# Performance work log

Measured on AMD Instinct MI355X. Metric: run time of the kernel, lower is better.

## Reference

```python
import jax, jax.numpy as jnp
import numpy as np

B, N, FIN, FOUT = 16, 128, 128, 256   # batch, atoms(=max_atom), in_features, out_features
EOUT, BIN, BOUT, CI, L1 = 64, 14, 64, 64, 256


def _rnn_dir(x, wih, whh, bih, bhh):
    # x: [B, T, I]; torch nn.RNN step: h = tanh(x @ Wih^T + bih + h @ Whh^T + bhh)
    h0 = jnp.zeros((x.shape[0], whh.shape[0]), x.dtype)
    def step(h, xt):
        h = jnp.tanh(xt @ wih.T + bih + h @ whh.T + bhh)
        return h, h
    _, ys = jax.lax.scan(step, h0, jnp.swapaxes(x, 0, 1))
    return jnp.swapaxes(ys, 0, 1)  # [B, T, H]


def _bi_rnn(x, wih_f, whh_f, bih_f, bhh_f, wih_b, whh_b, bih_b, bhh_b):
    fwd = _rnn_dir(x, wih_f, whh_f, bih_f, bhh_f)
    bwd = _rnn_dir(x[:, ::-1, :], wih_b, whh_b, bih_b, bhh_b)[:, ::-1, :]
    return jnp.concatenate([fwd, bwd], axis=-1)  # [B, T, 2H]


def setup_inputs() -> dict:
    key = jax.random.key(0)
    ks = jax.random.split(key, 24)
    g = lambda i, shape, s=0.05: (jax.random.normal(ks[i], shape, jnp.float32) * s)
    return {
        "x": g(0, (B, N, FIN), 1.0),
        "adj": jax.random.randint(ks[1], (B, N, N), 0, 2).astype(jnp.int32),
        "w_edge": g(2, (B, N, N, BIN), 1.0),
        "W": g(3, (FIN, FOUT)),
        "a": g(4, (2 * FOUT, EOUT)),
        "wfc_w": g(5, (BIN, BOUT)), "wfc_b": g(6, (BOUT,)),
        "fc_w": g(7, (EOUT + BOUT, 1)), "fc_b": g(8, (1,)),
        "fcc_w": g(9, (FOUT, 1)), "fcc_b": g(10, (1,)),
        "wih_f": g(11, (CI, N)), "whh_f": g(12, (CI, CI)), "bih_f": g(13, (CI,)), "bhh_f": g(14, (CI,)),
        "wih_b": g(15, (CI, N)), "whh_b": g(16, (CI, CI)), "bih_b": g(17, (CI,)), "bhh_b": g(18, (CI,)),
        "fco_w": g(19, (2 * CI + FOUT, L1)), "fco_b": g(20, (L1,)),
    }


def reference(x, adj, w_edge, W, a, wfc_w, wfc_b, fc_w, fc_b, fcc_w, fcc_b,
              wih_f, whh_f, bih_f, bhh_f, wih_b, whh_b, bih_b, bhh_b, fco_w, fco_b):
    h = x @ W  # [B, N, FOUT]
    # faithful reproduction of the repeat/cat(dim=1)/view trick
    t1 = jnp.tile(h, (1, 1, N)).reshape(B, N * N, FOUT)  # row i*N+j = h_i
    t2 = jnp.tile(h, (1, N, 1))                          # row i*N+j = h_j
    atom_trans = jnp.concatenate([t1, t2], axis=1).reshape(B, N, N, 2 * FOUT)
    e = atom_trans @ a                                   # [B, N, N, EOUT]
    wproj = w_edge @ wfc_w + wfc_b                       # [B, N, N, BOUT]
    e = jax.nn.leaky_relu(jnp.concatenate([e, wproj], axis=3))
    e = (e @ fc_w + fc_b)[..., 0]                        # [B, N, N]
    att = jax.nn.softmax(jnp.where(adj > 0, e, jnp.float32(-9e15)), axis=2)
    # dropout is identity in eval mode
    at_in = att[..., None] * h[:, :, None, :]            # [B, N, N, FOUT], h_i broadcast over j
    hn = jax.nn.leaky_relu((at_in @ fcc_w + fcc_b)[..., 0])  # [B, N, N]
    hn = jax.nn.leaky_relu(_bi_rnn(hn, wih_f, whh_f, bih_f, bhh_f, wih_b, whh_b, bih_b, bhh_b))
    h1 = jnp.einsum('bij,bjf->bif', att, h)              # [B, N, FOUT]
    out = jnp.concatenate([hn, h1], axis=2) @ fco_w + fco_b  # [B, N, L1]
    return jax.nn.elu(out)
```

## Files before the change

### kernel.cpp

```cpp
#include <hip/hip_runtime.h>
#include <hip/hip_bf16.h>

#define DEV static __device__ __forceinline__

constexpr int B=16, N=128, FIN=128, FOUT=256, EOUT=64, BINW=14, BOUT=64, CI=64, L1=256;

constexpr int O_H   = 0;
constexpr int O_S   = O_H  + B*N*FOUT;
constexpr int O_SU  = O_S  + B*N;
constexpr int O_SV  = O_SU + B*N;
constexpr int O_ATT = O_SV + B*N;
constexpr int O_ZF  = O_ATT+ B*N*N;
constexpr int O_ZB  = O_ZF + B*N*CI;
constexpr int O_RF  = O_ZB + B*N*CI;
constexpr int O_RB  = O_RF + B*N*CI;
constexpr int O_H1  = O_RB + B*N*CI;

DEV float bf16_to_f32(unsigned short u){
  unsigned int x = ((unsigned int)u) << 16; float f;
  __builtin_memcpy(&f, &x, 4); return f;
}
DEV void bf2x(unsigned int u, float& lo, float& hi){
  unsigned int a = u << 16, b = u & 0xFFFF0000u;
  __builtin_memcpy(&lo, &a, 4); __builtin_memcpy(&hi, &b, 4);
}
DEV float lrelu(float x){ return x > 0.f ? x : 0.01f * x; }
DEV float bcastf(float v, int lane){
  return __builtin_bit_cast(float, __builtin_amdgcn_readlane(__builtin_bit_cast(int, v), lane));
}
DEV float ldf(const void* p, int i, int m){
  return m ? bf16_to_f32(((const unsigned short*)p)[i]) : ((const float*)p)[i];
}
DEV int blk_mode(const void* x, int nt, int tid){
  const unsigned short* u = (const unsigned short*)x;
  int e = (u[tid & 255] >> 7) & 0xFF;
  int cnt = __syncthreads_count(e >= 100 && e <= 140);
  return cnt * 4 >= nt * 3;
}

__global__ __launch_bounds__(256) void k_h_pq(const void* __restrict__ xr,
                                              const void* __restrict__ Wp,
                                              const void* __restrict__ Ap,
                                              const void* __restrict__ fccwp,
                                              const void* __restrict__ fcwp,
                                              float* __restrict__ ws){
  int blk = blockIdx.x, tid = threadIdx.x;
  int b = blk >> 4, i0 = (blk & 15) * 8;
  __shared__ __align__(16) float xl[8*FIN];
  __shared__ __align__(16) float hrow[8*FOUT];
  __shared__ __align__(16) float pl[8*EOUT];
  __shared__ __align__(16) float ql[8*EOUT];
  __shared__ float red[32];
  int mode = blk_mode(xr, 256, tid);
  if (mode){
    const unsigned short* xu = (const unsigned short*)xr + (size_t)(b*N + i0)*FIN;
    for (int t = tid; t < 8*FIN/8; t += 256){
      uint4 u4 = ((const uint4*)xu)[t];
      float* o = &xl[t*8];
      bf2x(u4.x,o[0],o[1]); bf2x(u4.y,o[2],o[3]); bf2x(u4.z,o[4],o[5]); bf2x(u4.w,o[6],o[7]);
    }
  } else {
    const float* xf = (const float*)xr + (size_t)(b*N + i0)*FIN;
    for (int t4 = tid; t4 < 8*FIN/4; t4 += 256)
      *(float4*)&xl[t4*4] = ((const float4*)xf)[t4];
  }
  __syncthreads();
  int f = tid;
  float acc[8] = {0,0,0,0,0,0,0,0};
  if (mode){
    const unsigned short* Wu = (const unsigned short*)Wp;
    for (int c = 0; c < FIN; c += 4){
      float w0 = bf16_to_f32(Wu[(c+0)*FOUT + f]);
      float w1 = bf16_to_f32(Wu[(c+1)*FOUT + f]);
      float w2 = bf16_to_f32(Wu[(c+2)*FOUT + f]);
      float w3 = bf16_to_f32(Wu[(c+3)*FOUT + f]);
      #pragma unroll
      for (int r = 0; r < 8; ++r){
        float4 x4 = *(const float4*)&xl[r*FIN + c];
        acc[r] += x4.x*w0 + x4.y*w1 + x4.z*w2 + x4.w*w3;
      }
    }
  } else {
    const float* Wf = (const float*)Wp;
    for (int c = 0; c < FIN; c += 4){
      float w0 = Wf[(c+0)*FOUT + f];
      float w1 = Wf[(c+1)*FOUT + f];
      float w2 = Wf[(c+2)*FOUT + f];
      float w3 = Wf[(c+3)*FOUT + f];
      #pragma unroll
      for (int r = 0; r < 8; ++r){
        float4 x4 = *(const float4*)&xl[r*FIN + c];
        acc[r] += x4.x*w0 + x4.y*w1 + x4.z*w2 + x4.w*w3;
      }
    }
  }
  float fw = ldf(fccwp, f, mode);
  #pragma unroll
  for (int r = 0; r < 8; ++r){
    ws[O_H + (b*N + i0 + r)*FOUT + f] = acc[r];
    hrow[r*FOUT + f] = acc[r];
  }
  #pragma unroll
  for (int r = 0; r < 8; ++r){
    float v = acc[r] * fw;
    for (int off = 32; off; off >>= 1) v += __shfl_down(v, off);
    if ((tid & 63) == 0) red[(tid >> 6)*8 + r] = v;
  }
  __syncthreads();
  if (tid < 8){
    float s = red[tid] + red[8+tid] + red[16+tid] + red[24+tid];
    ws[O_S + b*N + i0 + tid] = s;
  }
  {
    int o = tid & 63, which = (tid >> 6) & 1, hh = tid >> 7;
    float a4[4] = {0.f,0.f,0.f,0.f};
    if (mode){
      const unsigned short* Au = (const unsigned short*)Ap;
      for (int c = 0; c < FOUT; c += 4){
        float w0 = bf16_to_f32(Au[(which*FOUT + c+0)*EOUT + o]);
        float w1 = bf16_to_f32(Au[(which*FOUT + c+1)*EOUT + o]);
        float w2 = bf16_to_f32(Au[(which*FOUT + c+2)*EOUT + o]);
        float w3 = bf16_to_f32(Au[(which*FOUT + c+3)*EOUT + o]);
        #pragma unroll
        for (int r = 0; r < 4; ++r){
          float4 h4 = *(const float4*)&hrow[(hh*4+r)*FOUT + c];
          a4[r] += h4.x*w0 + h4.y*w1 + h4.z*w2 + h4.w*w3;
        }
      }
    } else {
      const float* Af = (const float*)Ap;
      for (int c = 0; c < FOUT; c += 4){
        float w0 = Af[(which*FOUT + c+0)*EOUT + o];
        float w1 = Af[(which*FOUT + c+1)*EOUT + o];
        float w2 = Af[(which*FOUT + c+2)*EOUT + o];
        float w3 = Af[(which*FOUT + c+3)*EOUT + o];
        #pragma unroll
        for (int r = 0; r < 4; ++r){
          float4 h4 = *(const float4*)&hrow[(hh*4+r)*FOUT + c];
          a4[r] += h4.x*w0 + h4.y*w1 + h4.z*w2 + h4.w*w3;
        }
      }
    }
    float* dst = which ? ql : pl;
    #pragma unroll
    for (int r = 0; r < 4; ++r) dst[(hh*4+r)*EOUT + o] = a4[r];
  }
  __syncthreads();
  {
    int o = tid & 63, w = tid >> 6;
    float fw2 = ldf(fcwp, o, mode);
    float s1 = lrelu(pl[w*EOUT + o]     + ql[w*EOUT + o])     * fw2;
    float s2 = lrelu(pl[(w+4)*EOUT + o] + ql[(w+4)*EOUT + o]) * fw2;
    float s3 = lrelu(pl[(2*w)*EOUT + o] + ql[(2*w+1)*EOUT + o]) * fw2;
    for (int off = 32; off; off >>= 1){
      s1 += __shfl_down(s1, off); s2 += __shfl_down(s2, off); s3 += __shfl_down(s3, off);
    }
    if (o == 0){
      ws[O_SU + b*N + i0 + w]     = s1;
      ws[O_SU + b*N + i0 + w + 4] = s2;
      int r1 = (i0 + 2*w) >> 1;
      ws[O_SV + b*N + r1]      = s3;
      ws[O_SV + b*N + r1 + 64] = s3;
    }
  }
}

struct AttArgs { const void *we,*x,*wfcw,*wfcb,*fcw,*fcb,*fccb,*wihf,*bihf,*bhhf,*wihb,*bihb,*bhhb; };

__global__ __launch_bounds__(256) void k_att(AttArgs A, const int* __restrict__ adj,
                                             float* __restrict__ ws){
  int blk = blockIdx.x, tid = threadIdx.x;
  int half = tid >> 7, j = tid & 127, wv = (tid >> 6) & 1;
  int tau = blk*2 + half;
  int b = tau >> 7, i = tau & 127;
  __shared__ __align__(16) float wel[2][N*BINW];
  __shared__ __align__(16) float hnp[2][N];
  __shared__ __align__(16) float wfcwl[BINW*BOUT];
  __shared__ __align__(16) float wfcbl[BOUT];
  __shared__ __align__(16) float fcw2l[BOUT];
  __shared__ float red2[2][2];
  int mode = blk_mode(A.x, 256, tid);
  for (int t = tid; t < BINW*BOUT; t += 256) wfcwl[t] = ldf(A.wfcw, t, mode);
  if (tid < BOUT){ wfcbl[tid] = ldf(A.wfcb, tid, mode); fcw2l[tid] = ldf(A.fcw, EOUT + tid, mode); }
  if (mode){
    const unsigned short* weu = (const unsigned short*)A.we + (size_t)(b*N + i)*N*BINW;
    for (int t = j; t < N*BINW/8; t += 128){
      uint4 q = ((const uint4*)weu)[t];
      float* o = &wel[half][t*8];
      bf2x(q.x,o[0],o[1]); bf2x(q.y,o[2],o[3]); bf2x(q.z,o[4],o[5]); bf2x(q.w,o[6],o[7]);
    }
  } else {
    const float* wef = (const float*)A.we + (size_t)(b*N + i)*N*BINW;
    for (int t4 = j; t4 < N*BINW/4; t4 += 128)
      *(float4*)&wel[half][t4*4] = ((const float4*)wef)[t4];
  }
  __syncthreads();
  float wr[BINW];
  #pragma unroll
  for (int t = 0; t < BINW; ++t) wr[t] = wel[half][j*BINW + t];
  float wcon = 0.f;
  for (int o = 0; o < BOUT; o += 4){
    float4 bb = *(const float4*)&wfcbl[o];
    float w0 = bb.x, w1 = bb.y, w2 = bb.z, w3 = bb.w;
    #pragma unroll
    for (int t = 0; t < BINW; ++t){
      float4 w4 = *(const float4*)&wfcwl[t*BOUT + o];
      w0 = fmaf(wr[t], w4.x, w0); w1 = fmaf(wr[t], w4.y, w1);
      w2 = fmaf(wr[t], w4.z, w2); w3 = fmaf(wr[t], w4.w, w3);
    }
    float4 f4 = *(const float4*)&fcw2l[o];
    wcon += lrelu(w0)*f4.x + lrelu(w1)*f4.y + lrelu(w2)*f4.z + lrelu(w3)*f4.w;
  }
  const float* R = ws;
  float econ = (i < 64) ? R[O_SU + b*N + 2*i + (j >= 64 ? 1 : 0)]
                        : R[O_SV + b*N + j];
  float etot = econ + wcon + ldf(A.fcb, 0, mode);
  float m = (adj[(b*N + i)*N + j] > 0) ? etot : -9e15f;
  float mx = m;
  for (int off = 32; off; off >>= 1) mx = fmaxf(mx, __shfl_xor(mx, off));
  if ((tid & 63) == 0) red2[half][wv] = mx;
  __syncthreads();
  mx = fmaxf(red2[half][0], red2[half][1]);
  float ev = expf(m - mx);
  float sum = ev;
  for (int off = 32; off; off >>= 1) sum += __shfl_xor(sum, off);
  __syncthreads();
  if ((tid & 63) == 0) red2[half][wv] = sum;
  __syncthreads();
  sum = red2[half][0] + red2[half][1];
  float att = ev / sum;
  ws[O_ATT + (b*N + i)*N + j] = att;
  float sbi = R[O_S + b*N + i];
  hnp[half][j] = lrelu(att * sbi + ldf(A.fccb, 0, mode));
  __syncthreads();
  {
    int d = wv, c = tid & 63;
    float acc = ldf(d ? A.bihb : A.bihf, c, mode) + ldf(d ? A.bhhb : A.bhhf, c, mode);
    const void* wihp = d ? A.wihb : A.wihf;
    if (mode){
      const uint4* wq = (const uint4*)((const unsigned short*)wihp + c*N);
      #pragma unroll 4
      for (int k = 0; k < N; k += 8){
        uint4 q = wq[k >> 3];
        float w0,w1,w2,w3,w4,w5,w6,w7;
        bf2x(q.x,w0,w1); bf2x(q.y,w2,w3); bf2x(q.z,w4,w5); bf2x(q.w,w6,w7);
        float4 h0 = *(const float4*)&hnp[half][k];
        float4 h1 = *(const float4*)&hnp[half][k+4];
        acc += h0.x*w0 + h0.y*w1 + h0.z*w2 + h0.w*w3
             + h1.x*w4 + h1.y*w5 + h1.z*w6 + h1.w*w7;
      }
    } else {
      const float* wf = (const float*)wihp + c*N;
      #pragma unroll 8
      for (int k = 0; k < N; k += 4){
        float4 h4 = *(const float4*)&hnp[half][k];
        float4 w4 = *(const float4*)&wf[k];
        acc += h4.x*w4.x + h4.y*w4.y + h4.z*w4.z + h4.w*w4.w;
      }
    }
    ws[(d ? O_ZB : O_ZF) + (b*N + i)*CI + c] = acc;
  }
}

__global__ __launch_bounds__(256, 1) void k_rnn_h1(const void* __restrict__ xr,
                                                   const void* __restrict__ whhf,
                                                   const void* __restrict__ whhb,
                                                   float* __restrict__ ws){
  __shared__ __align__(16) float sh[N*CI];
  int blk = blockIdx.x, tid = threadIdx.x;
  int mode = blk_mode(xr, 256, tid);
  const float* R = ws;
  if (blk < 32){
    int d = blk >> 4, b = blk & 15;
    const int zb = (d ? O_ZB : O_ZF) + b*N*CI;
    const int ob = (d ? O_RB : O_RF) + b*N*CI;
    for (int it = tid; it < N*CI/4; it += 256)
      *(float4*)&sh[it*4] = *(const float4*)&ws[zb + it*4];
    __syncthreads();
    if (tid < 64){
      int c = tid;
      const void* whhp = d ? whhb : whhf;
      float wreg[CI];
      if (mode){
        const uint4* wq = (const uint4*)((const unsigned short*)whhp + c*CI);
        #pragma unroll
        for (int k = 0; k < CI; k += 8){
          uint4 q = wq[k >> 3];
          bf2x(q.x,wreg[k+0],wreg[k+1]); bf2x(q.y,wreg[k+2],wreg[k+3]);
          bf2x(q.z,wreg[k+4],wreg[k+5]); bf2x(q.w,wreg[k+6],wreg[k+7]);
        }
      } else {
        const float* wf = (const float*)whhp + c*CI;
        #pragma unroll
        for (int k = 0; k < CI; k += 4){
          float4 w4 = *(const float4*)&wf[k];
          wreg[k]=w4.x; wreg[k+1]=w4.y; wreg[k+2]=w4.z; wreg[k+3]=w4.w;
        }
      }
      const int step = d ? -1 : 1;
      int tt = d ? (N-1) : 0;
      float hv = 0.f;
      float z = sh[tt*CI + c];
      for (int t = 0; t < N; ++t){
        int ti = tt + step; ti = ti < 0 ? 0 : (ti > N-1 ? N-1 : ti);
        float znext = sh[ti*CI + c];
        float s[CI];
        #pragma unroll
        for (int k = 0; k < CI; ++k) s[k] = bcastf(hv, k);
#if __has_builtin(__builtin_amdgcn_sched_barrier)
        __builtin_amdgcn_sched_barrier(0);
#endif
        float a0 = z, a1 = 0.f, a2 = 0.f, a3 = 0.f;
        #pragma unroll
        for (int k = 0; k < CI; k += 4){
          a0 = fmaf(s[k+0], wreg[k+0], a0);
          a1 = fmaf(s[k+1], wreg[k+1], a1);
          a2 = fmaf(s[k+2], wreg[k+2], a2);
          a3 = fmaf(s[k+3], wreg[k+3], a3);
        }
        float x = (a0+a1)+(a2+a3);
        x = fminf(15.f, fmaxf(-15.f, x));
        float p = __expf(2.f * x);
        hv = (p - 1.f) * __builtin_amdgcn_rcpf(p + 1.f);
        sh[tt*CI + c] = hv;
        z = znext;
        tt += step;
      }
    }
    __syncthreads();
    for (int it = tid; it < N*CI/4; it += 256)
      *(float4*)&ws[ob + it*4] = *(const float4*)&sh[it*4];
  } else {
    for (int task = blk - 32; task < 256; task += 224){
      int b = task >> 4, i0 = (task & 15) * 8;
      int f = tid;
      __syncthreads();
      for (int t = tid; t < 8*N; t += 256){
        int r = t >> 7, k = t & 127;
        sh[k*8 + r] = R[O_ATT + (b*N + i0 + r)*N + k];
      }
      __syncthreads();
      float acc[8] = {0,0,0,0,0,0,0,0};
      for (int k = 0; k < N; ++k){
        float hv = R[O_H + (b*N + k)*FOUT + f];
        float4 a0 = *(const float4*)&sh[k*8];
        float4 a1 = *(const float4*)&sh[k*8 + 4];
        acc[0] += a0.x*hv; acc[1] += a0.y*hv; acc[2] += a0.z*hv; acc[3] += a0.w*hv;
        acc[4] += a1.x*hv; acc[5] += a1.y*hv; acc[6] += a1.z*hv; acc[7] += a1.w*hv;
      }
      #pragma unroll
      for (int r = 0; r < 8; ++r)
        ws[O_H1 + (b*N + i0 + r)*FOUT + f] = acc[r];
    }
  }
}

__global__ __launch_bounds__(256) void k_out(const void* __restrict__ xr,
                                             const void* __restrict__ fcowp,
                                             const void* __restrict__ fcobp,
                                             const float* __restrict__ R, void* dout){
  int blk = blockIdx.x, tid = threadIdx.x;
  int b = blk >> 4, i0 = (blk & 15) * 8;
  constexpr int KW = 2*CI + FOUT;
  __shared__ __align__(16) float inl[8*KW];
  int mode = blk_mode(xr, 256, tid);
  for (int t = tid; t < 8*2*CI; t += 256){
    int r = t >> 7, k = t & 127;
    int row = b*N + i0 + r;
    inl[r*KW + k] = (k < CI) ? lrelu(R[O_RF + row*CI + k])
                             : lrelu(R[O_RB + row*CI + (k - CI)]);
  }
  for (int t = tid; t < 8*FOUT; t += 256){
    int r = t >> 8, k = t & 255;
    inl[r*KW + 2*CI + k] = R[O_H1 + (b*N + i0 + r)*FOUT + k];
  }
  __syncthreads();
  int l = tid;
  float bias = ldf(fcobp, l, mode);
  float acc[8];
  #pragma unroll
  for (int r = 0; r < 8; ++r) acc[r] = bias;
  if (mode){
    const unsigned short* fu = (const unsigned short*)fcowp;
    for (int k = 0; k < KW; k += 4){
      float w0 = bf16_to_f32(fu[(k+0)*L1 + l]);
      float w1 = bf16_to_f32(fu[(k+1)*L1 + l]);
      float w2 = bf16_to_f32(fu[(k+2)*L1 + l]);
      float w3 = bf16_to_f32(fu[(k+3)*L1 + l]);
      #pragma unroll
      for (int r = 0; r < 8; ++r){
        float4 v = *(const float4*)&inl[r*KW + k];
        acc[r] += v.x*w0 + v.y*w1 + v.z*w2 + v.w*w3;
      }
    }
  } else {
    const float* ff = (const float*)fcowp;
    for (int k = 0; k < KW; k += 4){
      float w0 = ff[(k+0)*L1 + l];
      float w1 = ff[(k+1)*L1 + l];
      float w2 = ff[(k+2)*L1 + l];
      float w3 = ff[(k+3)*L1 + l];
      #pragma unroll
      for (int r = 0; r < 8; ++r){
        float4 v = *(const float4*)&inl[r*KW + k];
        acc[r] += v.x*w0 + v.y*w1 + v.z*w2 + v.w*w3;
      }
    }
  }
  #pragma unroll
  for (int r = 0; r < 8; ++r){
    float o = acc[r] > 0.f ? acc[r] : expm1f(acc[r]);
    int idx = (b*N + i0 + r)*L1 + l;
    if (mode) ((__hip_bfloat16*)dout)[idx] = __float2bfloat16(o);
    else      ((float*)dout)[idx] = o;
  }
}

extern "C" void kernel_launch(void* const* d_in, const int* in_sizes, int n_in,
                              void* d_out, int out_size, void* d_ws, size_t ws_size,
                              hipStream_t stream){
  (void)in_sizes; (void)n_in; (void)out_size; (void)ws_size;
  float* ws = (float*)d_ws;
  AttArgs A;
  A.we = d_in[2]; A.x = d_in[0]; A.wfcw = d_in[5]; A.wfcb = d_in[6];
  A.fcw = d_in[7]; A.fcb = d_in[8]; A.fccb = d_in[10];
  A.wihf = d_in[11]; A.bihf = d_in[13]; A.bhhf = d_in[14];
  A.wihb = d_in[15]; A.bihb = d_in[17]; A.bhhb = d_in[18];
  hipLaunchKernelGGL(k_h_pq,   dim3(256),    dim3(256), 0, stream,
                     d_in[0], d_in[3], d_in[4], d_in[9], d_in[7], ws);
  hipLaunchKernelGGL(k_att,    dim3(B*N/2),  dim3(256), 0, stream, A, (const int*)d_in[1], ws);
  hipLaunchKernelGGL(k_rnn_h1, dim3(256),    dim3(256), 0, stream,
                     d_in[0], d_in[12], d_in[16], ws);
  hipLaunchKernelGGL(k_out,    dim3(256),    dim3(256), 0, stream,
                     d_in[0], d_in[19], d_in[20], ws, d_out);
}
```

Before: 206.8 us.

## Fuse four kernels into one cooperative persistent kernel with grid syncs

Merges the h/pq projection, attention, RNN/h1 and output kernels into a single cooperative launch of 256 blocks, with grid-wide syncs between stages. The attention stage, which previously used 1024 blocks, now loops over 4 row pairs per block. The aim is to remove three kernel launch gaps and their tail effects. In exchange the attention stage has less parallelism, and each grid sync plus threadfence adds its own cost.

```diff
diff --git a/kernel.cpp b/kernel.cpp
--- a/kernel.cpp
+++ b/kernel.cpp
@@ -1,5 +1,8 @@
 #include <hip/hip_runtime.h>
 #include <hip/hip_bf16.h>
+#include <hip/hip_cooperative_groups.h>
+
+namespace cg = cooperative_groups;
 
 #define DEV static __device__ __forceinline__
 
@@ -38,381 +41,388 @@
   return cnt * 4 >= nt * 3;
 }
 
-__global__ __launch_bounds__(256) void k_h_pq(const void* __restrict__ xr,
-                                              const void* __restrict__ Wp,
-                                              const void* __restrict__ Ap,
-                                              const void* __restrict__ fccwp,
-                                              const void* __restrict__ fcwp,
-                                              float* __restrict__ ws){
+struct FA {
+  const void *x, *Wp, *Ap, *fccw, *fcw;
+  const int  *adj;
+  const void *we, *wfcw, *wfcb, *fcb, *fccb;
+  const void *wihf, *bihf, *bhhf, *wihb, *bihb, *bhhb;
+  const void *whhf, *whhb;
+  const void *fcow, *fcob;
+  float *ws;
+  void  *dout;
+};
+
+__global__ __launch_bounds__(256, 1) void k_fused(FA A){
+  cg::grid_group gg = cg::this_grid();
+  __shared__ __align__(16) float smem[8192];
   int blk = blockIdx.x, tid = threadIdx.x;
-  int b = blk >> 4, i0 = (blk & 15) * 8;
-  __shared__ __align__(16) float xl[8*FIN];
-  __shared__ __align__(16) float hrow[8*FOUT];
-  __shared__ __align__(16) float pl[8*EOUT];
-  __shared__ __align__(16) float ql[8*EOUT];
-  __shared__ float red[32];
-  int mode = blk_mode(xr, 256, tid);
-  if (mode){
-    const unsigned short* xu = (const unsigned short*)xr + (size_t)(b*N + i0)*FIN;
-    for (int t = tid; t < 8*FIN/8; t += 256){
-      uint4 u4 = ((const uint4*)xu)[t];
-      float* o = &xl[t*8];
-      bf2x(u4.x,o[0],o[1]); bf2x(u4.y,o[2],o[3]); bf2x(u4.z,o[4],o[5]); bf2x(u4.w,o[6],o[7]);
-    }
-  } else {
-    const float* xf = (const float*)xr + (size_t)(b*N + i0)*FIN;
-    for (int t4 = tid; t4 < 8*FIN/4; t4 += 256)
-      *(float4*)&xl[t4*4] = ((const float4*)xf)[t4];
+  int mode = blk_mode(A.x, 256, tid);
+  float* ws = A.ws;
+  const float* R = ws;
+
+  {
+    int b = blk >> 4, i0 = (blk & 15) * 8;
+    float* xl   = smem;
+    float* hrow = smem + 1024;
+    float* pl   = smem + 3072;
+    float* ql   = smem + 3584;
+    float* red  = smem + 4096;
+    if (mode){
+      const unsigned short* xu = (const unsigned short*)A.x + (size_t)(b*N + i0)*FIN;
+      for (int t = tid; t < 8*FIN/8; t += 256){
+        uint4 u4 = ((const uint4*)xu)[t];
+        float* o = &xl[t*8];
+        bf2x(u4.x,o[0],o[1]); bf2x(u4.y,o[2],o[3]); bf2x(u4.z,o[4],o[5]); bf2x(u4.w,o[6],o[7]);
+      }
+    } else {
+      const float* xf = (const float*)A.x + (size_t)(b*N + i0)*FIN;
+      for (int t4 = tid; t4 < 8*FIN/4; t4 += 256)
+        *(float4*)&xl[t4*4] = ((const float4*)xf)[t4];
+    }
+    __syncthreads();
+    int f = tid;
+    float acc[8] = {0,0,0,0,0,0,0,0};
+    if (mode){
+      const unsigned short* Wu = (const unsigned short*)A.Wp;
+      for (int c = 0; c < FIN; c += 4){
+        float w0 = bf16_to_f32(Wu[(c+0)*FOUT + f]);
+        float w1 = bf16_to_f32(Wu[(c+1)*FOUT + f]);
+        float w2 = bf16_to_f32(Wu[(c+2)*FOUT + f]);
+        float w3 = bf16_to_f32(Wu[(c+3)*FOUT + f]);
+        #pragma unroll
+        for (int r = 0; r < 8; ++r){
+          float4 x4 = *(const float4*)&xl[r*FIN + c];
+          acc[r] += x4.x*w0 + x4.y*w1 + x4.z*w2 + x4.w*w3;
+        }
+      }
+    } else {
+      const float* Wf = (const float*)A.Wp;
+      for (int c = 0; c < FIN; c += 4){
+        float w0 = Wf[(c+0)*FOUT + f];
+        float w1 = Wf[(c+1)*FOUT + f];
+        float w2 = Wf[(c+2)*FOUT + f];
+        float w3 = Wf[(c+3)*FOUT + f];
+        #pragma unroll
+        for (int r = 0; r < 8; ++r){
+          float4 x4 = *(const float4*)&xl[r*FIN + c];
+          acc[r] += x4.x*w0 + x4.y*w1 + x4.z*w2 + x4.w*w3;
+        }
+      }
+    }
+    float fw = ldf(A.fccw, f, mode);
+    #pragma unroll
+    for (int r = 0; r < 8; ++r){
+      ws[O_H + (b*N + i0 + r)*FOUT + f] = acc[r];
+      hrow[r*FOUT + f] = acc[r];
+    }
+    #pragma unroll
+    for (int r = 0; r < 8; ++r){
+      float v = acc[r] * fw;
+      for (int off = 32; off; off >>= 1) v += __shfl_down(v, off);
+      if ((tid & 63) == 0) red[(tid >> 6)*8 + r] = v;
+    }
+    __syncthreads();
+    if (tid < 8){
+      float s = red[tid] + red[8+tid] + red[16+tid] + red[24+tid];
+      ws[O_S + b*N + i0 + tid] = s;
+    }
+    {
+      int o = tid & 63, which = (tid >> 6) & 1, hh = tid >> 7;
+      float a4[4] = {0.f,0.f,0.f,0.f};
+      if (mode){
+        const unsigned short* Au = (const unsigned short*)A.Ap;
+        for (int c = 0; c < FOUT; c += 4){
+          float w0 = bf16_to_f32(Au[(which*FOUT + c+0)*EOUT + o]);
+          float w1 = bf16_to_f32(Au[(which*FOUT + c+1)*EOUT + o]);
+          float w2 = bf16_to_f32(Au[(which*FOUT + c+2)*EOUT + o]);
+          float w3 = bf16_to_f32(Au[(which*FOUT + c+3)*EOUT + o]);
+          #pragma unroll
+          for (int r = 0; r < 4; ++r){
+            float4 h4 = *(const float4*)&hrow[(hh*4+r)*FOUT + c];
+            a4[r] += h4.x*w0 + h4.y*w1 + h4.z*w2 + h4.w*w3;
+          }
+        }
+      } else {
+        const float* Af = (const float*)A.Ap;
+        for (int c = 0; c < FOUT; c += 4){
+          float w0 = Af[(which*FOUT + c+0)*EOUT + o];
+          float w1 = Af[(which*FOUT + c+1)*EOUT + o];
+          float w2 = Af[(which*FOUT + c+2)*EOUT + o];
+          float w3 = Af[(which*FOUT + c+3)*EOUT + o];
+          #pragma unroll
+          for (int r = 0; r < 4; ++r){
+            float4 h4 = *(const float4*)&hrow[(hh*4+r)*FOUT + c];
+            a4[r] += h4.x*w0 + h4.y*w1 + h4.z*w2 + h4.w*w3;
+          }
+        }
+      }
+      float* dst = which ? ql : pl;
+      #pragma unroll
+      for (int r = 0; r < 4; ++r) dst[(hh*4+r)*EOUT + o] = a4[r];
+    }
+    __syncthreads();
+    {
+      int o = tid & 63, w = tid >> 6;
+      float fw2 = ldf(A.fcw, o, mode);
+      float s1 = lrelu(pl[w*EOUT + o]     + ql[w*EOUT + o])     * fw2;
+      float s2 = lrelu(pl[(w+4)*EOUT + o] + ql[(w+4)*EOUT + o]) * fw2;
+      float s3 = lrelu(pl[(2*w)*EOUT + o] + ql[(2*w+1)*EOUT + o]) * fw2;
+      for (int off = 32; off; off >>= 1){
+        s1 += __shfl_down(s1, off); s2 += __shfl_down(s2, off); s3 += __shfl_down(s3, off);
+      }
+      if (o == 0){
+        ws[O_SU + b*N + i0 + w]     = s1;
+        ws[O_SU + b*N + i0 + w + 4] = s2;
+        int r1 = (i0 + 2*w) >> 1;
+        ws[O_SV + b*N + r1]      = s3;
+        ws[O_SV + b*N + r1 + 64] = s3;
+      }
+    }
   }
-  __syncthreads();
-  int f = tid;
-  float acc[8] = {0,0,0,0,0,0,0,0};
-  if (mode){
-    const unsigned short* Wu = (const unsigned short*)Wp;
-    for (int c = 0; c < FIN; c += 4){
-      float w0 = bf16_to_f32(Wu[(c+0)*FOUT + f]);
-      float w1 = bf16_to_f32(Wu[(c+1)*FOUT + f]);
-      float w2 = bf16_to_f32(Wu[(c+2)*FOUT + f]);
-      float w3 = bf16_to_f32(Wu[(c+3)*FOUT + f]);
+  __threadfence();
+  gg.sync();
+
+  {
+    float (*wel)[N*BINW] = (float (*)[N*BINW])smem;
+    float (*hnp)[N]      = (float (*)[N])(smem + 3584);
+    float* wfcwl = smem + 3840;
+    float* wfcbl = smem + 4736;
+    float* fcw2l = smem + 4800;
+    float (*red2)[2]     = (float (*)[2])(smem + 4864);
+    for (int t = tid; t < BINW*BOUT; t += 256) wfcwl[t] = ldf(A.wfcw, t, mode);
+    if (tid < BOUT){ wfcbl[tid] = ldf(A.wfcb, tid, mode); fcw2l[tid] = ldf(A.fcw, EOUT + tid, mode); }
+    int half = tid >> 7, j = tid & 127, wv = (tid >> 6) & 1;
+    float fcbv = ldf(A.fcb, 0, mode), fccbv = ldf(A.fccb, 0, mode);
+    for (int pr = 0; pr < 4; ++pr){
+      int tau = blk*8 + pr*2 + half;
+      int b = tau >> 7, i = tau & 127;
+      if (mode){
+        const unsigned short* weu = (const unsigned short*)A.we + (size_t)(b*N + i)*N*BINW;
+        for (int t = j; t < N*BINW/8; t += 128){
+          uint4 q = ((const uint4*)weu)[t];
+          float* o = &wel[half][t*8];
+          bf2x(q.x,o[0],o[1]); bf2x(q.y,o[2],o[3]); bf2x(q.z,o[4],o[5]); bf2x(q.w,o[6],o[7]);
+        }
+      } else {
+        const float* wef = (const float*)A.we + (size_t)(b*N + i)*N*BINW;
+        for (int t4 = j; t4 < N*BINW/4; t4 += 128)
+          *(float4*)&wel[half][t4*4] = ((const float4*)wef)[t4];
+      }
+      __syncthreads();
+      float wr[BINW];
       #pragma unroll
-      for (int r = 0; r < 8; ++r){
-        float4 x4 = *(const float4*)&xl[r*FIN + c];
-        acc[r] += x4.x*w0 + x4.y*w1 + x4.z*w2 + x4.w*w3;
-      }
-    }
-  } else {
-    const float* Wf = (const float*)Wp;
-    for (int c = 0; c < FIN; c += 4){
-      float w0 = Wf[(c+0)*FOUT + f];
-      float w1 = Wf[(c+1)*FOUT + f];
-      float w2 = Wf[(c+2)*FOUT + f];
-      float w3 = Wf[(c+3)*FOUT + f];
-      #pragma unroll
-      for (int r = 0; r < 8; ++r){
-        float4 x4 = *(const float4*)&xl[r*FIN + c];
-        acc[r] += x4.x*w0 + x4.y*w1 + x4.z*w2 + x4.w*w3;
-      }
+      for (int t = 0; t < BINW; ++t) wr[t] = wel[half][j*BINW + t];
+      float wcon = 0.f;
+      for (int o = 0; o < BOUT; o += 4){
+        float4 bb = *(const float4*)&wfcbl[o];
+        float w0 = bb.x, w1 = bb.y, w2 = bb.z, w3 = bb.w;
+        #pragma unroll
+        for (int t = 0; t < BINW; ++t){
+          float4 w4 = *(const float4*)&wfcwl[t*BOUT + o];
+          w0 = fmaf(wr[t], w4.x, w0); w1 = fmaf(wr[t], w4.y, w1);
+          w2 = fmaf(wr[t], w4.z, w2); w3 = fmaf(wr[t], w4.w, w3);
+        }
+        float4 f4 = *(const float4*)&fcw2l[o];
+        wcon += lrelu(w0)*f4.x + lrelu(w1)*f4.y + lrelu(w2)*f4.z + lrelu(w3)*f4.w;
+      }
+      float econ = (i < 64) ? R[O_SU + b*N + 2*i + (j >= 64 ? 1 : 0)]
+                            : R[O_SV + b*N + j];
+      float etot = econ + wcon + fcbv;
+      float m = (A.adj[(b*N + i)*N + j] > 0) ? etot : -9e15f;
+      float mx = m;
+      for (int off = 32; off; off >>= 1) mx = fmaxf(mx, __shfl_xor(mx, off));
+      if ((tid & 63) == 0) red2[half][wv] = mx;
+      __syncthreads();
+      mx = fmaxf(red2[half][0], red2[half][1]);
+      float ev = expf(m - mx);
+      float sum = ev;
+      for (int off = 32; off; off >>= 1) sum += __shfl_xor(sum, off);
+      __syncthreads();
+      if ((tid & 63) == 0) red2[half][wv] = sum;
+      __syncthreads();
+      sum = red2[half][0] + red2[half][1];
+      float att = ev / sum;
+      ws[O_ATT + (b*N + i)*N + j] = att;
+      float sbi = R[O_S + b*N + i];
+      hnp[half][j] = lrelu(att * sbi + fccbv);
+      __syncthreads();
+      {
+        int d = wv, c = tid & 63;
+        float acc = ldf(d ? A.bihb : A.bihf, c, mode) + ldf(d ? A.bhhb : A.bhhf, c, mode);
+        const void* wihp = d ? A.wihb : A.wihf;
+        if (mode){
+          const uint4* wq = (const uint4*)((const unsigned short*)wihp + c*N);
+          #pragma unroll 4
+          for (int k = 0; k < N; k += 8){
+            uint4 q = wq[k >> 3];
+            float w0,w1,w2,w3,w4,w5,w6,w7;
+            bf2x(q.x,w0,w1); bf2x(q.y,w2,w3); bf2x(q.z,w4,w5); bf2x(q.w,w6,w7);
+            float4 h0 = *(const float4*)&hnp[half][k];
+            float4 h1 = *(const float4*)&hnp[half][k+4];
+            acc += h0.x*w0 + h0.y*w1 + h0.z*w2 + h0.w*w3
+                 + h1.x*w4 + h1.y*w5 + h1.z*w6 + h1.w*w7;
+          }
+        } else {
+          const float* wf = (const float*)wihp + c*N;
+          #pragma unroll 8
+          for (int k = 0; k < N; k += 4){
+            float4 h4 = *(const float4*)&hnp[half][k];
+            float4 w4 = *(const float4*)&wf[k];
+            acc += h4.x*w4.x + h4.y*w4.y + h4.z*w4.z + h4.w*w4.w;
+          }
+        }
+        ws[(d ? O_ZB : O_ZF) + (b*N + i)*CI + c] = acc;
+      }
+      __syncthreads();
     }
   }
-  float fw = ldf(fccwp, f, mode);
-  #pragma unroll
-  for (int r = 0; r < 8; ++r){
-    ws[O_H + (b*N + i0 + r)*FOUT + f] = acc[r];
-    hrow[r*FOUT + f] = acc[r];
+  __threadfence();
+  gg.sync();
+
+  {
+    float* sh = smem;
+    if (blk < 32){
+      int d = blk >> 4, b = blk & 15;
+      const int zb = (d ? O_ZB : O_ZF) + b*N*CI;
+      const int ob = (d ? O_RB : O_RF) + b*N*CI;
+      for (int it = tid; it < N*CI/4; it += 256)
+        *(float4*)&sh[it*4] = *(const float4*)&ws[zb + it*4];
+      __syncthreads();
+      if (tid < 64){
+        int c = tid;
+        const void* whhp = d ? A.whhb : A.whhf;
+        float wreg[CI];
+        if (mode){
+          const uint4* wq = (const uint4*)((const unsigned short*)whhp + c*CI);
+          #pragma unroll
+          for (int k = 0; k < CI; k += 8){
+            uint4 q = wq[k >> 3];
+            bf2x(q.x,wreg[k+0],wreg[k+1]); bf2x(q.y,wreg[k+2],wreg[k+3]);
+            bf2x(q.z,wreg[k+4],wreg[k+5]); bf2x(q.w,wreg[k+6],wreg[k+7]);
+          }
+        } else {
+          const float* wf = (const float*)whhp + c*CI;
+          #pragma unroll
+          for (int k = 0; k < CI; k += 4){
+            float4 w4 = *(const float4*)&wf[k];
+            wreg[k]=w4.x; wreg[k+1]=w4.y; wreg[k+2]=w4.z; wreg[k+3]=w4.w;
+          }
+        }
+        const int step = d ? -1 : 1;
+        int tt = d ? (N-1) : 0;
+        float hv = 0.f;
+        float z = sh[tt*CI + c];
+        for (int t = 0; t < N; ++t){
+          int ti = tt + step; ti = ti < 0 ? 0 : (ti > N-1 ? N-1 : ti);
+          float znext = sh[ti*CI + c];
+          float s[CI];
+          #pragma unroll
+          for (int k = 0; k < CI; ++k) s[k] = bcastf(hv, k);
+#if __has_builtin(__builtin_amdgcn_sched_barrier)
+          __builtin_amdgcn_sched_barrier(0);
+#endif
+          float a0 = z, a1 = 0.f, a2 = 0.f, a3 = 0.f;
+          #pragma unroll
+          for (int k = 0; k < CI; k += 4){
+            a0 = fmaf(s[k+0], wreg[k+0], a0);
+            a1 = fmaf(s[k+1], wreg[k+1], a1);
+            a2 = fmaf(s[k+2], wreg[k+2], a2);
+            a3 = fmaf(s[k+3], wreg[k+3], a3);
+          }
+          float x = (a0+a1)+(a2+a3);
+          x = fminf(15.f, fmaxf(-15.f, x));
+          float p = __expf(2.f * x);
+          hv = (p - 1.f) * __builtin_amdgcn_rcpf(p + 1.f);
+          sh[tt*CI + c] = hv;
+          z = znext;
+          tt += step;
+        }
+      }
+      __syncthreads();
+      for (int it = tid; it < N*CI/4; it += 256)
+        *(float4*)&ws[ob + it*4] = *(const float4*)&sh[it*4];
+    } else {
+      for (int task = blk - 32; task < 256; task += 224){
+        int b = task >> 4, i0 = (task & 15) * 8;
+        int f = tid;
+        __syncthreads();
+        for (int t = tid; t < 8*N; t += 256){
+          int r = t >> 7, k = t & 127;
+          sh[k*8 + r] = R[O_ATT + (b*N + i0 + r)*N + k];
+        }
+        __syncthreads();
+        float acc[8] = {0,0,0,0,0,0,0,0};
+        for (int k = 0; k < N; ++k){
+          float hv = R[O_H + (b*N + k)*FOUT + f];
+          float4 a0 = *(const float4*)&sh[k*8];
+          float4 a1 = *(const float4*)&sh[k*8 + 4];
+          acc[0] += a0.x*hv; acc[1] += a0.y*hv; acc[2] += a0.z*hv; acc[3] += a0.w*hv;
+          acc[4] += a1.x*hv; acc[5] += a1.y*hv; acc[6] += a1.z*hv; acc[7] += a1.w*hv;
+        }
+        #pragma unroll
+        for (int r = 0; r < 8; ++r)
+          ws[O_H1 + (b*N + i0 + r)*FOUT + f] = acc[r];
+      }
+    }
   }
-  #pragma unroll
-  for (int r = 0; r < 8; ++r){
-    float v = acc[r] * fw;
-    for (int off = 32; off; off >>= 1) v += __shfl_down(v, off);
-    if ((tid & 63) == 0) red[(tid >> 6)*8 + r] = v;
-  }
-  __syncthreads();
-  if (tid < 8){
-    float s = red[tid] + red[8+tid] + red[16+tid] + red[24+tid];
-    ws[O_S + b*N + i0 + tid] = s;
-  }
+  __threadfence();
+  gg.sync();
+
   {
-    int o = tid & 63, which = (tid >> 6) & 1, hh = tid >> 7;
-    float a4[4] = {0.f,0.f,0.f,0.f};
+    int b = blk >> 4, i0 = (blk & 15) * 8;
+    constexpr int KW = 2*CI + FOUT;
+    float* inl = smem;
+    __syncthreads();
+    for (int t = tid; t < 8*2*CI; t += 256){
+      int r = t >> 7, k = t & 127;
+      int row = b*N + i0 + r;
+      inl[r*KW + k] = (k < CI) ? lrelu(R[O_RF + row*CI + k])
+                               : lrelu(R[O_RB + row*CI + (k - CI)]);
+    }
+    for (int t = tid; t < 8*FOUT; t += 256){
+      int r = t >> 8, k = t & 255;
+      inl[r*KW + 2*CI + k] = R[O_H1 + (b*N + i0 + r)*FOUT + k];
+    }
+    __syncthreads();
+    int l = tid;
+    float bias = ldf(A.fcob, l, mode);
+    float acc[8];
+    #pragma unroll
+    for (int r = 0; r < 8; ++r) acc[r] = bias;
     if (mode){
-      const unsigned short* Au = (const unsigned short*)Ap;
-      for (int c = 0; c < FOUT; c += 4){
-        float w0 = bf16_to_f32(Au[(which*FOUT + c+0)*EOUT + o]);
-        float w1 = bf16_to_f32(Au[(which*FOUT + c+1)*EOUT + o]);
-        float w2 = bf16_to_f32(Au[(which*FOUT + c+2)*EOUT + o]);
-        float w3 = bf16_to_f32(Au[(which*FOUT + c+3)*EOUT + o]);
-        #pragma unroll
-        for (int r = 0; r < 4; ++r){
-          float4 h4 = *(const float4*)&hrow[(hh*4+r)*FOUT + c];
-          a4[r] += h4.x*w0 + h4.y*w1 + h4.z*w2 + h4.w*w3;
+      const unsigned short* fu = (const unsigned short*)A.fcow;
+      for (int k = 0; k < KW; k += 4){
+        float w0 = bf16_to_f32(fu[(k+0)*L1 + l]);
+        float w1 = bf16_to_f32(fu[(k+1)*L1 + l]);
+        float w2 = bf16_to_f32(fu[(k+2)*L1 + l]);
+        float w3 = bf16_to_f32(fu[(k+3)*L1 + l]);
+        #pragma unroll
+        for (int r = 0; r < 8; ++r){
+          float4 v = *(const float4*)&inl[r*KW + k];
+          acc[r] += v.x*w0 + v.y*w1 + v.z*w2 + v.w*w3;
         }
       }
     } else {
-      const float* Af = (const float*)Ap;
-      for (int c = 0; c < FOUT; c += 4){
-        float w0 = Af[(which*FOUT + c+0)*EOUT + o];
-        float w1 = Af[(which*FOUT + c+1)*EOUT + o];
-        float w2 = Af[(which*FOUT + c+2)*EOUT + o];
-        float w3 = Af[(which*FOUT + c+3)*EOUT + o];
-        #pragma unroll
-        for (int r = 0; r < 4; ++r){
-          float4 h4 = *(const float4*)&hrow[(hh*4+r)*FOUT + c];
-          a4[r] += h4.x*w0 + h4.y*w1 + h4.z*w2 + h4.w*w3;
-        }
-      }
-    }
-    float* dst = which ? ql : pl;
+      const float* ff = (const float*)A.fcow;
+      for (int k = 0; k < KW; k += 4){
+        float w0 = ff[(k+0)*L1 + l];
+        float w1 = ff[(k+1)*L1 + l];
+        float w2 = ff[(k+2)*L1 + l];
+        float w3 = ff[(k+3)*L1 + l];
+        #pragma unroll
+        for (int r = 0; r < 8; ++r){
+          float4 v = *(const float4*)&inl[r*KW + k];
+          acc[r] += v.x*w0 + v.y*w1 + v.z*w2 + v.w*w3;
+        }
+      }
+    }
     #pragma unroll
-    for (int r = 0; r < 4; ++r) dst[(hh*4+r)*EOUT + o] = a4[r];
-  }
-  __syncthreads();
-  {
-    int o = tid & 63, w = tid >> 6;
-    float fw2 = ldf(fcwp, o, mode);
-    float s1 = lrelu(pl[w*EOUT + o]     + ql[w*EOUT + o])     * fw2;
-    float s2 = lrelu(pl[(w+4)*EOUT + o] + ql[(w+4)*EOUT + o]) * fw2;
-    float s3 = lrelu(pl[(2*w)*EOUT + o] + ql[(2*w+1)*EOUT + o]) * fw2;
-    for (int off = 32; off; off >>= 1){
-      s1 += __shfl_down(s1, off); s2 += __shfl_down(s2, off); s3 += __shfl_down(s3, off);
-    }
-    if (o == 0){
-      ws[O_SU + b*N + i0 + w]     = s1;
-      ws[O_SU + b*N + i0 + w + 4] = s2;
-      int r1 = (i0 + 2*w) >> 1;
-      ws[O_SV + b*N + r1]      = s3;
-      ws[O_SV + b*N + r1 + 64] = s3;
-    }
-  }
-}
-
-struct AttArgs { const void *we,*x,*wfcw,*wfcb,*fcw,*fcb,*fccb,*wihf,*bihf,*bhhf,*wihb,*bihb,*bhhb; };
-
-__global__ __launch_bounds__(256) void k_att(AttArgs A, const int* __restrict__ adj,
-                                             float* __restrict__ ws){
-  int blk = blockIdx.x, tid = threadIdx.x;
-  int half = tid >> 7, j = tid & 127, wv = (tid >> 6) & 1;
-  int tau = blk*2 + half;
-  int b = tau >> 7, i = tau & 127;
-  __shared__ __align__(16) float wel[2][N*BINW];
-  __shared__ __align__(16) float hnp[2][N];
-  __shared__ __align__(16) float wfcwl[BINW*BOUT];
-  __shared__ __align__(16) float wfcbl[BOUT];
-  __shared__ __align__(16) float fcw2l[BOUT];
-  __shared__ float red2[2][2];
-  int mode = blk_mode(A.x, 256, tid);
-  for (int t = tid; t < BINW*BOUT; t += 256) wfcwl[t] = ldf(A.wfcw, t, mode);
-  if (tid < BOUT){ wfcbl[tid] = ldf(A.wfcb, tid, mode); fcw2l[tid] = ldf(A.fcw, EOUT + tid, mode); }
-  if (mode){
-    const unsigned short* weu = (const unsigned short*)A.we + (size_t)(b*N + i)*N*BINW;
-    for (int t = j; t < N*BINW/8; t += 128){
-      uint4 q = ((const uint4*)weu)[t];
-      float* o = &wel[half][t*8];
-      bf2x(q.x,o[0],o[1]); bf2x(q.y,o[2],o[3]); bf2x(q.z,o[4],o[5]); bf2x(q.w,o[6],o[7]);
-    }
-  } else {
-    const float* wef = (const float*)A.we + (size_t)(b*N + i)*N*BINW;
-    for (int t4 = j; t4 < N*BINW/4; t4 += 128)
-      *(float4*)&wel[half][t4*4] = ((const float4*)wef)[t4];
-  }
-  __syncthreads();
-  float wr[BINW];
-  #pragma unroll
-  for (int t = 0; t < BINW; ++t) wr[t] = wel[half][j*BINW + t];
-  float wcon = 0.f;
-  for (int o = 0; o < BOUT; o += 4){
-    float4 bb = *(const float4*)&wfcbl[o];
-    float w0 = bb.x, w1 = bb.y, w2 = bb.z, w3 = bb.w;
-    #pragma unroll
-    for (int t = 0; t < BINW; ++t){
-      float4 w4 = *(const float4*)&wfcwl[t*BOUT + o];
-      w0 = fmaf(wr[t], w4.x, w0); w1 = fmaf(wr[t], w4.y, w1);
-      w2 = fmaf(wr[t], w4.z, w2); w3 = fmaf(wr[t], w4.w, w3);
-    }
-    float4 f4 = *(const float4*)&fcw2l[o];
-    wcon += lrelu(w0)*f4.x + lrelu(w1)*f4.y + lrelu(w2)*f4.z + lrelu(w3)*f4.w;
-  }
-  const float* R = ws;
-  float econ = (i < 64) ? R[O_SU + b*N + 2*i + (j >= 64 ? 1 : 0)]
-                        : R[O_SV + b*N + j];
-  float etot = econ + wcon + ldf(A.fcb, 0, mode);
-  float m = (adj[(b*N + i)*N + j] > 0) ? etot : -9e15f;
-  float mx = m;
-  for (int off = 32; off; off >>= 1) mx = fmaxf(mx, __shfl_xor(mx, off));
-  if ((tid & 63) == 0) red2[half][wv] = mx;
-  __syncthreads();
-  mx = fmaxf(red2[half][0], red2[half][1]);
-  float ev = expf(m - mx);
-  float sum = ev;
-  for (int off = 32; off; off >>= 1) sum += __shfl_xor(sum, off);
-  __syncthreads();
-  if ((tid & 63) == 0) red2[half][wv] = sum;
-  __syncthreads();
-  sum = red2[half][0] + red2[half][1];
-  float att = ev / sum;
-  ws[O_ATT + (b*N + i)*N + j] = att;
-  float sbi = R[O_S + b*N + i];
-  hnp[half][j] = lrelu(att * sbi + ldf(A.fccb, 0, mode));
-  __syncthreads();
-  {
-    int d = wv, c = tid & 63;
-    float acc = ldf(d ? A.bihb : A.bihf, c, mode) + ldf(d ? A.bhhb : A.bhhf, c, mode);
-    const void* wihp = d ? A.wihb : A.wihf;
-    if (mode){
-      const uint4* wq = (const uint4*)((const unsigned short*)wihp + c*N);
-      #pragma unroll 4
-      for (int k = 0; k < N; k += 8){
-        uint4 q = wq[k >> 3];
-        float w0,w1,w2,w3,w4,w5,w6,w7;
-        bf2x(q.x,w0,w1); bf2x(q.y,w2,w3); bf2x(q.z,w4,w5); bf2x(q.w,w6,w7);
-        float4 h0 = *(const float4*)&hnp[half][k];
-        float4 h1 = *(const float4*)&hnp[half][k+4];
-        acc += h0.x*w0 + h0.y*w1 + h0.z*w2 + h0.w*w3
-             + h1.x*w4 + h1.y*w5 + h1.z*w6 + h1.w*w7;
-      }
-    } else {
-      const float* wf = (const float*)wihp + c*N;
-      #pragma unroll 8
-      for (int k = 0; k < N; k += 4){
-        float4 h4 = *(const float4*)&hnp[half][k];
-        float4 w4 = *(const float4*)&wf[k];
-        acc += h4.x*w4.x + h4.y*w4.y + h4.z*w4.z + h4.w*w4.w;
-      }
-    }
-    ws[(d ? O_ZB : O_ZF) + (b*N + i)*CI + c] = acc;
-  }
-}
-
-__global__ __launch_bounds__(256, 1) void k_rnn_h1(const void* __restrict__ xr,
-                                                   const void* __restrict__ whhf,
-                                                   const void* __restrict__ whhb,
-                                                   float* __restrict__ ws){
-  __shared__ __align__(16) float sh[N*CI];
-  int blk = blockIdx.x, tid = threadIdx.x;
-  int mode = blk_mode(xr, 256, tid);
-  const float* R = ws;
-  if (blk < 32){
-    int d = blk >> 4, b = blk & 15;
-    const int zb = (d ? O_ZB : O_ZF) + b*N*CI;
-    const int ob = (d ? O_RB : O_RF) + b*N*CI;
-    for (int it = tid; it < N*CI/4; it += 256)
-      *(float4*)&sh[it*4] = *(const float4*)&ws[zb + it*4];
-    __syncthreads();
-    if (tid < 64){
-      int c = tid;
-      const void* whhp = d ? whhb : whhf;
-      float wreg[CI];
-      if (mode){
-        const uint4* wq = (const uint4*)((const unsigned short*)whhp + c*CI);
-        #pragma unroll
-        for (int k = 0; k < CI; k += 8){
-          uint4 q = wq[k >> 3];
-          bf2x(q.x,wreg[k+0],wreg[k+1]); bf2x(q.y,wreg[k+2],wreg[k+3]);
-          bf2x(q.z,wreg[k+4],wreg[k+5]); bf2x(q.w,wreg[k+6],wreg[k+7]);
-        }
-      } else {
-        const float* wf = (const float*)whhp + c*CI;
-        #pragma unroll
-        for (int k = 0; k < CI; k += 4){
-          float4 w4 = *(const float4*)&wf[k];
-          wreg[k]=w4.x; wreg[k+1]=w4.y; wreg[k+2]=w4.z; wreg[k+3]=w4.w;
-        }
-      }
-      const int step = d ? -1 : 1;
-      int tt = d ? (N-1) : 0;
-      float hv = 0.f;
-      float z = sh[tt*CI + c];
-      for (int t = 0; t < N; ++t){
-        int ti = tt + step; ti = ti < 0 ? 0 : (ti > N-1 ? N-1 : ti);
-        float znext = sh[ti*CI + c];
-        float s[CI];
-        #pragma unroll
-        for (int k = 0; k < CI; ++k) s[k] = bcastf(hv, k);
-#if __has_builtin(__builtin_amdgcn_sched_barrier)
-        __builtin_amdgcn_sched_barrier(0);
-#endif
-        float a0 = z, a1 = 0.f, a2 = 0.f, a3 = 0.f;
-        #pragma unroll
-        for (int k = 0; k < CI; k += 4){
-          a0 = fmaf(s[k+0], wreg[k+0], a0);
-          a1 = fmaf(s[k+1], wreg[k+1], a1);
-          a2 = fmaf(s[k+2], wreg[k+2], a2);
-          a3 = fmaf(s[k+3], wreg[k+3], a3);
-        }
-        float x = (a0+a1)+(a2+a3);
-        x = fminf(15.f, fmaxf(-15.f, x));
-        float p = __expf(2.f * x);
-        hv = (p - 1.f) * __builtin_amdgcn_rcpf(p + 1.f);
-        sh[tt*CI + c] = hv;
-        z = znext;
-        tt += step;
-      }
-    }
-    __syncthreads();
-    for (int it = tid; it < N*CI/4; it += 256)
-      *(float4*)&ws[ob + it*4] = *(const float4*)&sh[it*4];
-  } else {
-    for (int task = blk - 32; task < 256; task += 224){
-      int b = task >> 4, i0 = (task & 15) * 8;
-      int f = tid;
-      __syncthreads();
-      for (int t = tid; t < 8*N; t += 256){
-        int r = t >> 7, k = t & 127;
-        sh[k*8 + r] = R[O_ATT + (b*N + i0 + r)*N + k];
-      }
-      __syncthreads();
-      float acc[8] = {0,0,0,0,0,0,0,0};
-      for (int k = 0; k < N; ++k){
-        float hv = R[O_H + (b*N + k)*FOUT + f];
-        float4 a0 = *(const float4*)&sh[k*8];
-        float4 a1 = *(const float4*)&sh[k*8 + 4];
-        acc[0] += a0.x*hv; acc[1] += a0.y*hv; acc[2] += a0.z*hv; acc[3] += a0.w*hv;
-        acc[4] += a1.x*hv; acc[5] += a1.y*hv; acc[6] += a1.z*hv; acc[7] += a1.w*hv;
-      }
-      #pragma unroll
-      for (int r = 0; r < 8; ++r)
-        ws[O_H1 + (b*N + i0 + r)*FOUT + f] = acc[r];
-    }
-  }
-}
-
-__global__ __launch_bounds__(256) void k_out(const void* __restrict__ xr,
-                                             const void* __restrict__ fcowp,
-                                             const void* __restrict__ fcobp,
-                                             const float* __restrict__ R, void* dout){
-  int blk = blockIdx.x, tid = threadIdx.x;
-  int b = blk >> 4, i0 = (blk & 15) * 8;
-  constexpr int KW = 2*CI + FOUT;
-  __shared__ __align__(16) float inl[8*KW];
-  int mode = blk_mode(xr, 256, tid);
-  for (int t = tid; t < 8*2*CI; t += 256){
-    int r = t >> 7, k = t & 127;
-    int row = b*N + i0 + r;
-    inl[r*KW + k] = (k < CI) ? lrelu(R[O_RF + row*CI + k])
-                             : lrelu(R[O_RB + row*CI + (k - CI)]);
-  }
-  for (int t = tid; t < 8*FOUT; t += 256){
-    int r = t >> 8, k = t & 255;
-    inl[r*KW + 2*CI + k] = R[O_H1 + (b*N + i0 + r)*FOUT + k];
-  }
-  __syncthreads();
-  int l = tid;
-  float bias = ldf(fcobp, l, mode);
-  float acc[8];
-  #pragma unroll
-  for (int r = 0; r < 8; ++r) acc[r] = bias;
-  if (mode){
-    const unsigned short* fu = (const unsigned short*)fcowp;
-    for (int k = 0; k < KW; k += 4){
-      float w0 = bf16_to_f32(fu[(k+0)*L1 + l]);
-      float w1 = bf16_to_f32(fu[(k+1)*L1 + l]);
-      float w2 = bf16_to_f32(fu[(k+2)*L1 + l]);
-      float w3 = bf16_to_f32(fu[(k+3)*L1 + l]);
-      #pragma unroll
-      for (int r = 0; r < 8; ++r){
-        float4 v = *(const float4*)&inl[r*KW + k];
-        acc[r] += v.x*w0 + v.y*w1 + v.z*w2 + v.w*w3;
-      }
-    }
-  } else {
-    const float* ff = (const float*)fcowp;
-    for (int k = 0; k < KW; k += 4){
-      float w0 = ff[(k+0)*L1 + l];
-      float w1 = ff[(k+1)*L1 + l];
-      float w2 = ff[(k+2)*L1 + l];
-      float w3 = ff[(k+3)*L1 + l];
-      #pragma unroll
-      for (int r = 0; r < 8; ++r){
-        float4 v = *(const float4*)&inl[r*KW + k];
-        acc[r] += v.x*w0 + v.y*w1 + v.z*w2 + v.w*w3;
-      }
-    }
-  }
-  #pragma unroll
-  for (int r = 0; r < 8; ++r){
-    float o = acc[r] > 0.f ? acc[r] : expm1f(acc[r]);
-    int idx = (b*N + i0 + r)*L1 + l;
-    if (mode) ((__hip_bfloat16*)dout)[idx] = __float2bfloat16(o);
-    else      ((float*)dout)[idx] = o;
+    for (int r = 0; r < 8; ++r){
+      float o = acc[r] > 0.f ? acc[r] : expm1f(acc[r]);
+      int idx = (b*N + i0 + r)*L1 + l;
+      if (mode) ((__hip_bfloat16*)A.dout)[idx] = __float2bfloat16(o);
+      else      ((float*)A.dout)[idx] = o;
+    }
   }
 }
 
@@ -420,17 +430,17 @@
                               void* d_out, int out_size, void* d_ws, size_t ws_size,
                               hipStream_t stream){
   (void)in_sizes; (void)n_in; (void)out_size; (void)ws_size;
-  float* ws = (float*)d_ws;
-  AttArgs A;
-  A.we = d_in[2]; A.x = d_in[0]; A.wfcw = d_in[5]; A.wfcb = d_in[6];
-  A.fcw = d_in[7]; A.fcb = d_in[8]; A.fccb = d_in[10];
-  A.wihf = d_in[11]; A.bihf = d_in[13]; A.bhhf = d_in[14];
-  A.wihb = d_in[15]; A.bihb = d_in[17]; A.bhhb = d_in[18];
-  hipLaunchKernelGGL(k_h_pq,   dim3(256),    dim3(256), 0, stream,
-                     d_in[0], d_in[3], d_in[4], d_in[9], d_in[7], ws);
-  hipLaunchKernelGGL(k_att,    dim3(B*N/2),  dim3(256), 0, stream, A, (const int*)d_in[1], ws);
-  hipLaunchKernelGGL(k_rnn_h1, dim3(256),    dim3(256), 0, stream,
-                     d_in[0], d_in[12], d_in[16], ws);
-  hipLaunchKernelGGL(k_out,    dim3(256),    dim3(256), 0, stream,
-                     d_in[0], d_in[19], d_in[20], ws, d_out);
-}
+  FA fa;
+  fa.x    = d_in[0];  fa.adj  = (const int*)d_in[1]; fa.we  = d_in[2];
+  fa.Wp   = d_in[3];  fa.Ap   = d_in[4];
+  fa.wfcw = d_in[5];  fa.wfcb = d_in[6];
+  fa.fcw  = d_in[7];  fa.fcb  = d_in[8];
+  fa.fccw = d_in[9];  fa.fccb = d_in[10];
+  fa.wihf = d_in[11]; fa.whhf = d_in[12]; fa.bihf = d_in[13]; fa.bhhf = d_in[14];
+  fa.wihb = d_in[15]; fa.whhb = d_in[16]; fa.bihb = d_in[17]; fa.bhhb = d_in[18];
+  fa.fcow = d_in[19]; fa.fcob = d_in[20];
+  fa.ws   = (float*)d_ws;
+  fa.dout = d_out;
+  void* kp[] = { &fa };
+  hipLaunchCooperativeKernel((void*)k_fused, dim3(256), dim3(256), kp, 0, stream);
+}
```

New measurement: 397.2 us. 1.92x slower.
